# Kernel optimization log

Hardware: AMD Instinct MI355X
Metric: run time of the kernel (lower is better)

The kernel has to match this reference:

```python
import jax, jax.numpy as jnp
import numpy as np

NPOINT = 2048  # N // stride


def sqdist(a, b):
    # a: [B,M,3], b: [B,N,3] -> squared euclidean distances [B,M,N] (== cdist(...)**2)
    return (jnp.sum(a * a, -1)[:, :, None] + jnp.sum(b * b, -1)[:, None, :]
            - 2.0 * jnp.einsum('bmc,bnc->bmn', a, b))


def farthest_point_sample(xyz, npoint):
    # xyz [B,N,3] -> int32 [B,npoint]; deterministic start at point 0
    B, N, _ = xyz.shape

    def step(carry, _):
        distance, farthest = carry
        centroid = jnp.take_along_axis(xyz, farthest[:, None, None], axis=1)  # [B,1,3]
        d = jnp.sum((xyz - centroid) ** 2, -1)                                # [B,N]
        distance = jnp.minimum(distance, d)
        nxt = jnp.argmax(distance, -1).astype(jnp.int32)
        return (distance, nxt), farthest

    init = (jnp.full((B, N), 1e10, xyz.dtype), jnp.zeros((B,), jnp.int32))
    _, idx = jax.lax.scan(step, init, None, length=npoint)
    return idx.T  # [B, npoint]


def ball_query(radius, k, xyz, new_xyz):
    # faithful to torch ball_query: mask out-of-radius as N, sort indices, take first k,
    # replace padding with the first valid neighbor
    B, N, _ = xyz.shape
    sqd = sqdist(new_xyz, xyz)                                   # [B,S,N]
    gi = jnp.where(sqd > radius ** 2, N, jnp.arange(N, dtype=jnp.int32))
    gi = jnp.sort(gi, axis=-1)[:, :, :k]                         # [B,S,k]
    first = gi[:, :, :1]
    return jnp.where(gi == N, first, gi)


def three_interpolation(points, features, query):
    # points [B,S,3], features [B,D,S], query [B,N,3] -> [B,D,N]
    d = sqdist(query, points)                                    # [B,N,S]
    neg, idx = jax.lax.top_k(-d, 3)                              # 3 smallest dists
    w = 1.0 / (-neg + 1e-8)
    w = w / jnp.sum(w, -1, keepdims=True)                        # [B,N,3]
    g = jnp.take_along_axis(features[:, :, None, :], idx[:, None, :, :], axis=3)  # [B,D,N,3]
    return jnp.sum(g * w[:, None, :, :], -1)


def setup_inputs() -> dict:
    key = jax.random.key(0)
    k1, k2, k3, k4 = jax.random.split(key, 4)
    xyz = jax.random.uniform(k1, (4, 8192, 3), dtype=jnp.float32)
    features = jax.random.normal(k2, (4, 64, 8192), dtype=jnp.float32)
    W1 = jax.random.normal(k3, (128, 67), dtype=jnp.float32) * 0.05   # (3+64)->128 pointwise conv
    W2 = jax.random.normal(k4, (128, 192), dtype=jnp.float32) * 0.05  # (64+128)->128 pointwise conv
    return {"xyz": xyz, "features": features, "W1": W1, "W2": W2}


def reference(xyz, features, W1, W2):
    RADIUS, K = 0.2, 16
    # --- set abstraction (SABlock): FPS -> ball query -> group -> conv -> maxpool ---
    sidx = farthest_point_sample(xyz, NPOINT)                        # [B,S]
    new_xyz = jnp.take_along_axis(xyz, sidx[:, :, None], axis=1)     # [B,S,3]
    nidx = ball_query(RADIUS, K, xyz, new_xyz)                       # [B,S,K]
    gxyz = jnp.take_along_axis(xyz[:, None, :, :], nidx[:, :, :, None], axis=2)  # [B,S,K,3]
    rel = gxyz - new_xyz[:, :, None, :]                              # relative coords
    gfeat = jnp.take_along_axis(features[:, :, None, :], nidx[:, None, :, :], axis=3)  # [B,D,S,K]
    grouped = jnp.concatenate([rel.transpose(0, 3, 1, 2), gfeat], axis=1)  # [B,3+D,S,K]
    h = jax.nn.relu(jnp.einsum('od,bdsk->bosk', W1, grouped))
    sub_x = jnp.max(h, -1)                                           # [B,O,S]
    # --- feature propagation (UpBlock): 3-NN interpolation back to N -> concat -> conv ---
    lerp = three_interpolation(new_xyz, sub_x, xyz)                  # [B,O,N]
    cat = jnp.concatenate([features, lerp], axis=1)                  # [B,D+O,N]
    return jax.nn.relu(jnp.einsum('od,bdn->bon', W2, cat))           # [B,O,N]
```

## Files before the change

kernel.cpp:

```cpp
#include <hip/hip_runtime.h>
#include <hip/hip_bf16.h>

#define BATCH 4
#define NPTS  8192
#define NSAMP 2048
#define NK    16
#define CFEAT 64
#define CG    67
#define CO1   128
#define CCAT  192
#define CO2   128

#define DEV __device__ __forceinline__

DEV float n3(float x, float y, float z) {
    return __fadd_rn(__fadd_rn(__fmul_rn(x, x), __fmul_rn(y, y)), __fmul_rn(z, z));
}
DEV float dot3(float ax, float ay, float az, float bx, float by, float bz) {
    return __fmaf_rn(az, bz, __fmaf_rn(ay, by, __fmul_rn(ax, bx)));
}
DEV float sqd_expand(float an, float bn, float d) {
    return __fsub_rn(__fadd_rn(an, bn), __fmul_rn(2.0f, d));
}

__global__ __launch_bounds__(256) void transpose_kernel(const float* __restrict__ F,
                                                        float* __restrict__ T) {
    __shared__ float tile[64][65];
    const int b = blockIdx.y;
    const int n0 = blockIdx.x * 64;
    const int tx = threadIdx.x & 63, ty = threadIdx.x >> 6;
    const float* Fb = F + (size_t)b * CFEAT * NPTS;
    float* Tb = T + (size_t)b * NPTS * CFEAT;
#pragma unroll
    for (int i = 0; i < 16; i++) {
        int c = ty + i * 4;
        tile[c][tx] = Fb[(size_t)c * NPTS + n0 + tx];
    }
    __syncthreads();
#pragma unroll
    for (int i = 0; i < 16; i++) {
        int r = ty + i * 4;
        Tb[(size_t)(n0 + r) * CFEAT + tx] = tile[tx][r];
    }
}

__global__ __launch_bounds__(512) void fps_kernel(const float* __restrict__ xyz,
                                                  float* __restrict__ new_xyz) {
    const int b = blockIdx.x;
    const int t = threadIdx.x;
    const int lane = t & 63, wv = t >> 6;
    const float* X = xyz + (size_t)b * NPTS * 3;

    __shared__ float sx[NPTS], sy[NPTS], sz[NPTS];
    __shared__ unsigned long long wred[2][8];

    float px[16], py[16], pz[16], dist[16];
    {
        const float4* X4 = (const float4*)X;
#pragma unroll
        for (int g = 0; g < 4; g++) {
            float4 f0 = X4[t * 12 + g * 3 + 0];
            float4 f1 = X4[t * 12 + g * 3 + 1];
            float4 f2 = X4[t * 12 + g * 3 + 2];
            px[g*4+0] = f0.x; py[g*4+0] = f0.y; pz[g*4+0] = f0.z;
            px[g*4+1] = f0.w; py[g*4+1] = f1.x; pz[g*4+1] = f1.y;
            px[g*4+2] = f1.z; py[g*4+2] = f1.w; pz[g*4+2] = f2.x;
            px[g*4+3] = f2.y; py[g*4+3] = f2.z; pz[g*4+3] = f2.w;
        }
#pragma unroll
        for (int j = 0; j < 16; j++) {
            int p = t * 16 + j;
            sx[p] = px[j]; sy[p] = py[j]; sz[p] = pz[j];
            dist[j] = 1e10f;
        }
    }
    __syncthreads();

    float cx = sx[0], cy = sy[0], cz = sz[0];
    if (t == 0) {
        size_t o = (size_t)b * NSAMP * 3;
        new_xyz[o + 0] = cx; new_xyz[o + 1] = cy; new_xyz[o + 2] = cz;
    }

    int par = 0;
    for (int s = 1; s < NSAMP; s++) {
#pragma unroll
        for (int j = 0; j < 16; j++) {
            float dx = __fsub_rn(px[j], cx);
            float dy = __fsub_rn(py[j], cy);
            float dz = __fsub_rn(pz[j], cz);
            float d = __fadd_rn(__fadd_rn(__fmul_rn(dx, dx), __fmul_rn(dy, dy)),
                                __fmul_rn(dz, dz));
            dist[j] = fminf(dist[j], d);
        }
        float mx[8];
#pragma unroll
        for (int j = 0; j < 8; j++) mx[j] = fmaxf(dist[2*j], dist[2*j+1]);
#pragma unroll
        for (int j = 0; j < 4; j++) mx[j] = fmaxf(mx[2*j], mx[2*j+1]);
        mx[0] = fmaxf(mx[0], mx[1]);
        float bv = fmaxf(mx[0], fmaxf(mx[2], mx[3]));
        int bj = 15;
#pragma unroll
        for (int j = 14; j >= 0; --j) bj = (dist[j] == bv) ? j : bj;

        float wmax = bv;
#pragma unroll
        for (int off = 32; off > 0; off >>= 1)
            wmax = fmaxf(wmax, __shfl_xor(wmax, off));
        unsigned long long em = __ballot(bv == wmax);
        int wl = __ffsll(em) - 1;
        int lidx = t * 16 + bj;
        int widx = __shfl(lidx, wl);
        if (lane == 0)
            wred[par][wv] = ((unsigned long long)__float_as_uint(wmax) << 32)
                          | (unsigned int)(~widx);
        __syncthreads();

        unsigned long long r0 = wred[par][0], r1 = wred[par][1];
        unsigned long long r2 = wred[par][2], r3 = wred[par][3];
        unsigned long long r4 = wred[par][4], r5 = wred[par][5];
        unsigned long long r6 = wred[par][6], r7 = wred[par][7];
        if (r1 > r0) r0 = r1;
        if (r3 > r2) r2 = r3;
        if (r5 > r4) r4 = r5;
        if (r7 > r6) r6 = r7;
        if (r2 > r0) r0 = r2;
        if (r6 > r4) r4 = r6;
        if (r4 > r0) r0 = r4;
        int idx = (int)(~(unsigned int)(r0 & 0xFFFFFFFFull));

        cx = sx[idx]; cy = sy[idx]; cz = sz[idx];
        if (t == 0) {
            size_t o = ((size_t)b * NSAMP + s) * 3;
            new_xyz[o + 0] = cx; new_xyz[o + 1] = cy; new_xyz[o + 2] = cz;
        }
        par ^= 1;
    }
}

__global__ __launch_bounds__(256) void ballq_kernel(const float* __restrict__ xyz,
                                                    const float* __restrict__ new_xyz,
                                                    int* __restrict__ nidx) {
    const int wv = threadIdx.x >> 6, lane = threadIdx.x & 63;
    const int q = blockIdx.x * 4 + wv;
    const int b = q >> 11;
    const float* X = xyz + (size_t)b * NPTS * 3;
    const float* Q = new_xyz + (size_t)q * 3;
    const float qx = Q[0], qy = Q[1], qz = Q[2];
    const float an = n3(qx, qy, qz);

    __shared__ int nb[4][NK];
    int cnt = 0;
    for (int base = 0; base < NPTS && cnt < NK; base += 64) {
        int p = base + lane;
        float x = X[p * 3 + 0], y = X[p * 3 + 1], z = X[p * 3 + 2];
        float bn = n3(x, y, z);
        float dt = dot3(qx, qy, qz, x, y, z);
        float sq = sqd_expand(an, bn, dt);
        bool in = (sq <= 0.04f);
        unsigned long long m = __ballot(in);
        if (in) {
            int pos = cnt + (int)__popcll(m & ((1ull << lane) - 1ull));
            if (pos < NK) nb[wv][pos] = p;
        }
        cnt += (int)__popcll(m);
    }
    __syncthreads();
    if (lane < NK) {
        int c = cnt < NK ? cnt : NK;
        int v = (lane < c) ? nb[wv][lane] : nb[wv][0];
        nidx[(size_t)q * NK + lane] = v;
    }
}

__global__ __launch_bounds__(256) void group_mlp_kernel(const float* __restrict__ xyz,
                                                        const float* __restrict__ featT,
                                                        const float* __restrict__ new_xyz,
                                                        const int* __restrict__ nidx,
                                                        const float* __restrict__ W1,
                                                        float* __restrict__ subxT) {
    __shared__ float w1t[CG * CO1];
    for (int i = threadIdx.x; i < CG * CO1; i += 256) {
        int d = i >> 7, o = i & 127;
        w1t[i] = W1[(size_t)o * CG + d];
    }
    __syncthreads();
    const int lane = threadIdx.x & 63, wv = threadIdx.x >> 6;

    for (int q = blockIdx.x * 4 + wv; q < BATCH * NSAMP; q += gridDim.x * 4) {
        const int b = q >> 11;
        const float* Q = new_xyz + (size_t)q * 3;
        const float qx = Q[0], qy = Q[1], qz = Q[2];
        const int* NB = nidx + (size_t)q * NK;
        float m0 = 0.0f, m1 = 0.0f;
#pragma unroll 1
        for (int k = 0; k < NK; k++) {
            const int n = NB[k];
            const float* P = xyz + ((size_t)b * NPTS + n) * 3;
            float rx = P[0] - qx, ry = P[1] - qy, rz = P[2] - qz;
            float fv = featT[((size_t)b * NPTS + n) * CFEAT + lane];
            float a0 = fmaf(w1t[0 * CO1 + lane], rx,
                       fmaf(w1t[1 * CO1 + lane], ry, w1t[2 * CO1 + lane] * rz));
            float a1 = fmaf(w1t[0 * CO1 + 64 + lane], rx,
                       fmaf(w1t[1 * CO1 + 64 + lane], ry, w1t[2 * CO1 + 64 + lane] * rz));
#pragma unroll
            for (int d = 3; d < CG; d++) {
                float g = __shfl(fv, d - 3);
                a0 = fmaf(w1t[d * CO1 + lane], g, a0);
                a1 = fmaf(w1t[d * CO1 + 64 + lane], g, a1);
            }
            m0 = fmaxf(m0, a0);
            m1 = fmaxf(m1, a1);
        }
        subxT[(size_t)q * CO1 + lane] = m0;
        subxT[(size_t)q * CO1 + 64 + lane] = m1;
    }
}

DEV void ins3(float dd, int jj,
              float& d0, int& i0, float& d1, int& i1, float& d2, int& i2) {
    bool c2 = (dd < d2) || (dd == d2 && jj < i2);
    if (c2) { d2 = dd; i2 = jj; }
    bool c1 = (d2 < d1) || (d2 == d1 && i2 < i1);
    if (c1) { float tv = d1; int ti = i1; d1 = d2; i1 = i2; d2 = tv; i2 = ti; }
    bool c0 = (d1 < d0) || (d1 == d0 && i1 < i0);
    if (c0) { float tv = d0; int ti = i0; d0 = d1; i0 = i1; d1 = tv; i1 = ti; }
}

__global__ __launch_bounds__(256) void interp_w2_kernel(const float* __restrict__ xyz,
                                                        const float* __restrict__ new_xyz,
                                                        const float* __restrict__ featT,
                                                        const float* __restrict__ subxT,
                                                        const float* __restrict__ W2,
                                                        float* __restrict__ out) {
    __shared__ float w2t[CCAT * CO2];
    __shared__ float catb[4][CCAT];
    for (int i = threadIdx.x; i < CCAT * CO2; i += 256) {
        int d = i >> 7, o = i & 127;
        w2t[i] = W2[(size_t)o * CCAT + d];
    }
    __syncthreads();
    const int lane = threadIdx.x & 63, wv = threadIdx.x >> 6;

    for (int q = blockIdx.x * 4 + wv; q < BATCH * NPTS; q += gridDim.x * 4) {
        const int b = q >> 13, n = q & (NPTS - 1);
        const float* P = xyz + (size_t)q * 3;
        const float qx = P[0], qy = P[1], qz = P[2];
        const float an = n3(qx, qy, qz);

        float d0 = 1e30f, d1 = 1e30f, d2 = 1e30f;
        int i0 = 0x7fffffff, i1 = 0x7fffffff, i2 = 0x7fffffff;
        for (int j = lane; j < NSAMP; j += 64) {
            const float* C = new_xyz + ((size_t)b * NSAMP + j) * 3;
            float x = C[0], y = C[1], z = C[2];
            float bn = n3(x, y, z);
            float dt = dot3(qx, qy, qz, x, y, z);
            float dd = sqd_expand(an, bn, dt);
            ins3(dd, j, d0, i0, d1, i1, d2, i2);
        }
#pragma unroll
        for (int off = 32; off > 0; off >>= 1) {
            float e0 = __shfl_xor(d0, off); int f0 = __shfl_xor(i0, off);
            float e1 = __shfl_xor(d1, off); int f1 = __shfl_xor(i1, off);
            float e2 = __shfl_xor(d2, off); int f2 = __shfl_xor(i2, off);
            ins3(e0, f0, d0, i0, d1, i1, d2, i2);
            ins3(e1, f1, d0, i0, d1, i1, d2, i2);
            ins3(e2, f2, d0, i0, d1, i1, d2, i2);
        }
        float w0 = 1.0f / (d0 + 1e-8f);
        float w1 = 1.0f / (d1 + 1e-8f);
        float w2 = 1.0f / (d2 + 1e-8f);
        float sw = (w0 + w1) + w2;
        w0 /= sw; w1 /= sw; w2 /= sw;

        const float* S = subxT + (size_t)b * NSAMP * CO1;
        float L0 = S[(size_t)i0 * CO1 + lane] * w0
                 + S[(size_t)i1 * CO1 + lane] * w1
                 + S[(size_t)i2 * CO1 + lane] * w2;
        float L1 = S[(size_t)i0 * CO1 + 64 + lane] * w0
                 + S[(size_t)i1 * CO1 + 64 + lane] * w1
                 + S[(size_t)i2 * CO1 + 64 + lane] * w2;

        float fv = featT[((size_t)b * NPTS + n) * CFEAT + lane];
        catb[wv][lane] = fv;
        catb[wv][64 + lane] = L0;
        catb[wv][128 + lane] = L1;
        __builtin_amdgcn_s_waitcnt(0);

        float a0 = 0.0f, a1 = 0.0f;
#pragma unroll 8
        for (int d = 0; d < CCAT; d++) {
            float cv = catb[wv][d];
            a0 = fmaf(w2t[d * CO2 + lane], cv, a0);
            a1 = fmaf(w2t[d * CO2 + 64 + lane], cv, a1);
        }
        out[((size_t)b * CO2 + lane) * NPTS + n] = fmaxf(a0, 0.0f);
        out[((size_t)b * CO2 + 64 + lane) * NPTS + n] = fmaxf(a1, 0.0f);
    }
}

extern "C" void kernel_launch(void* const* d_in, const int* in_sizes, int n_in,
                              void* d_out, int out_size, void* d_ws, size_t ws_size,
                              hipStream_t stream) {
    const float* xyz      = (const float*)d_in[0];
    const float* features = (const float*)d_in[1];
    const float* W1       = (const float*)d_in[2];
    const float* W2       = (const float*)d_in[3];
    float* out = (float*)d_out;

    float* featT   = (float*)d_ws;
    float* new_xyz = featT + (size_t)BATCH * NPTS * CFEAT;
    int*   nidx    = (int*)(new_xyz + (size_t)BATCH * NSAMP * 3);
    float* subxT   = (float*)(nidx + (size_t)BATCH * NSAMP * NK);

    transpose_kernel<<<dim3(NPTS / 64, BATCH), 256, 0, stream>>>(features, featT);
    fps_kernel<<<BATCH, 512, 0, stream>>>(xyz, new_xyz);
    ballq_kernel<<<(BATCH * NSAMP) / 4, 256, 0, stream>>>(xyz, new_xyz, nidx);
    group_mlp_kernel<<<512, 256, 0, stream>>>(xyz, featT, new_xyz, nidx, W1, subxT);
    interp_w2_kernel<<<256, 256, 0, stream>>>(xyz, new_xyz, featT, subxT, W2, out);
}
```

Measured before the change: 2.834 ms.

## Spatially sort FPS points into grid cells and cull distance updates by bounding sphere

Points are bucketed into an 8x8x8 grid with a shared-memory counting sort, so each thread owns 16 spatially nearby points. Each thread keeps a bounding sphere and its current max min-distance, and skips the distance update when the new centroid is too far away to lower any of its distances. Whole waves whose lanes all skip reuse their cached packed max instead of redoing the shuffle reduction. This trades a one-time sort plus extra branches and registers for less per-iteration arithmetic in the serial FPS loop. Tie-breaking now takes the minimum original index through pid, which should preserve argmax semantics.

```diff
diff --git a/kernel.cpp b/kernel.cpp
--- a/kernel.cpp
+++ b/kernel.cpp
@@ -23,6 +23,13 @@
     return __fsub_rn(__fadd_rn(an, bn), __fmul_rn(2.0f, d));
 }
 
+DEV int cellof(float x, float y, float z) {
+    int ix = min(7, (int)(x * 8.0f));
+    int iy = min(7, (int)(y * 8.0f));
+    int iz = min(7, (int)(z * 8.0f));
+    return (iz << 6) | (iy << 3) | ix;
+}
+
 __global__ __launch_bounds__(256) void transpose_kernel(const float* __restrict__ F,
                                                         float* __restrict__ T) {
     __shared__ float tile[64][65];
@@ -52,9 +59,13 @@
     const float* X = xyz + (size_t)b * NPTS * 3;
 
     __shared__ float sx[NPTS], sy[NPTS], sz[NPTS];
+    __shared__ unsigned short sidx[NPTS];
+    __shared__ unsigned int cnt_off[512];
     __shared__ unsigned long long wred[2][8];
 
     float px[16], py[16], pz[16], dist[16];
+    int pid[16];
+
     {
         const float4* X4 = (const float4*)X;
 #pragma unroll
@@ -71,10 +82,58 @@
         for (int j = 0; j < 16; j++) {
             int p = t * 16 + j;
             sx[p] = px[j]; sy[p] = py[j]; sz[p] = pz[j];
-            dist[j] = 1e10f;
-        }
-    }
-    __syncthreads();
+        }
+    }
+    cnt_off[t] = 0;
+    __syncthreads();
+#pragma unroll
+    for (int j = 0; j < 16; j++)
+        atomicAdd(&cnt_off[cellof(px[j], py[j], pz[j])], 1u);
+    __syncthreads();
+    if (t < 64) {
+        unsigned h[8], lsum = 0;
+#pragma unroll
+        for (int k = 0; k < 8; k++) { h[k] = cnt_off[t * 8 + k]; lsum += h[k]; }
+        unsigned run = lsum;
+#pragma unroll
+        for (int d = 1; d < 64; d <<= 1) {
+            unsigned o = __shfl_up(run, d);
+            if (lane >= d) run += o;
+        }
+        unsigned acc = run - lsum;
+#pragma unroll
+        for (int k = 0; k < 8; k++) { cnt_off[t * 8 + k] = acc; acc += h[k]; }
+    }
+    __syncthreads();
+#pragma unroll
+    for (int j = 0; j < 16; j++) {
+        int c = cellof(px[j], py[j], pz[j]);
+        unsigned pos = atomicAdd(&cnt_off[c], 1u);
+        sidx[pos] = (unsigned short)(t * 16 + j);
+    }
+    __syncthreads();
+#pragma unroll
+    for (int j = 0; j < 16; j++) {
+        int p = sidx[t * 16 + j];
+        pid[j] = p;
+        px[j] = sx[p]; py[j] = sy[p]; pz[j] = sz[p];
+        dist[j] = 1e10f;
+    }
+    float mnx = px[0], mxx = px[0], mny = py[0], mxy = py[0], mnz = pz[0], mxz = pz[0];
+#pragma unroll
+    for (int j = 1; j < 16; j++) {
+        mnx = fminf(mnx, px[j]); mxx = fmaxf(mxx, px[j]);
+        mny = fminf(mny, py[j]); mxy = fmaxf(mxy, py[j]);
+        mnz = fminf(mnz, pz[j]); mxz = fmaxf(mxz, pz[j]);
+    }
+    const float rx = 0.5f * (mnx + mxx), ry = 0.5f * (mny + mxy), rz = 0.5f * (mnz + mxz);
+    float r2m = 0.0f;
+#pragma unroll
+    for (int j = 0; j < 16; j++) {
+        float dx = px[j] - rx, dy = py[j] - ry, dz = pz[j] - rz;
+        r2m = fmaxf(r2m, dx * dx + dy * dy + dz * dz);
+    }
+    const float rad = sqrtf(r2m) * 1.0001f + 1e-6f;
 
     float cx = sx[0], cy = sy[0], cz = sz[0];
     if (t == 0) {
@@ -82,39 +141,52 @@
         new_xyz[o + 0] = cx; new_xyz[o + 1] = cy; new_xyz[o + 2] = cz;
     }
 
+    float bv = 1e10f;
+    int bidx = 0;
+    float cullR = 3e38f;
+    unsigned long long wpack = 0;
+
     int par = 0;
     for (int s = 1; s < NSAMP; s++) {
-#pragma unroll
-        for (int j = 0; j < 16; j++) {
-            float dx = __fsub_rn(px[j], cx);
-            float dy = __fsub_rn(py[j], cy);
-            float dz = __fsub_rn(pz[j], cz);
-            float d = __fadd_rn(__fadd_rn(__fmul_rn(dx, dx), __fmul_rn(dy, dy)),
-                                __fmul_rn(dz, dz));
-            dist[j] = fminf(dist[j], d);
-        }
-        float mx[8];
-#pragma unroll
-        for (int j = 0; j < 8; j++) mx[j] = fmaxf(dist[2*j], dist[2*j+1]);
-#pragma unroll
-        for (int j = 0; j < 4; j++) mx[j] = fmaxf(mx[2*j], mx[2*j+1]);
-        mx[0] = fmaxf(mx[0], mx[1]);
-        float bv = fmaxf(mx[0], fmaxf(mx[2], mx[3]));
-        int bj = 15;
-#pragma unroll
-        for (int j = 14; j >= 0; --j) bj = (dist[j] == bv) ? j : bj;
-
-        float wmax = bv;
-#pragma unroll
-        for (int off = 32; off > 0; off >>= 1)
-            wmax = fmaxf(wmax, __shfl_xor(wmax, off));
-        unsigned long long em = __ballot(bv == wmax);
-        int wl = __ffsll(em) - 1;
-        int lidx = t * 16 + bj;
-        int widx = __shfl(lidx, wl);
-        if (lane == 0)
-            wred[par][wv] = ((unsigned long long)__float_as_uint(wmax) << 32)
-                          | (unsigned int)(~widx);
+        float ddx = cx - rx, ddy = cy - ry, ddz = cz - rz;
+        float dc2 = ddx * ddx + ddy * ddy + ddz * ddz;
+        bool upd = dc2 < cullR;
+        if (__ballot(upd) != 0) {
+            if (upd) {
+#pragma unroll
+                for (int j = 0; j < 16; j++) {
+                    float dx = __fsub_rn(px[j], cx);
+                    float dy = __fsub_rn(py[j], cy);
+                    float dz = __fsub_rn(pz[j], cz);
+                    float d = __fadd_rn(__fadd_rn(__fmul_rn(dx, dx), __fmul_rn(dy, dy)),
+                                        __fmul_rn(dz, dz));
+                    dist[j] = fminf(dist[j], d);
+                }
+                float m8[8];
+#pragma unroll
+                for (int j = 0; j < 8; j++) m8[j] = fmaxf(dist[j], dist[j + 8]);
+#pragma unroll
+                for (int j = 0; j < 4; j++) m8[j] = fmaxf(m8[j], m8[j + 4]);
+                bv = fmaxf(fmaxf(m8[0], m8[1]), fmaxf(m8[2], m8[3]));
+                int nb = 0x7fffffff;
+#pragma unroll
+                for (int j = 0; j < 16; j++)
+                    if (dist[j] == bv) nb = min(nb, pid[j]);
+                bidx = nb;
+                float sb = sqrtf(bv) * 1.0001f + 1e-6f;
+                float rr = rad + sb;
+                cullR = rr * rr;
+            }
+            unsigned long long pk = ((unsigned long long)__float_as_uint(bv) << 32)
+                                  | (unsigned int)(~bidx);
+#pragma unroll
+            for (int off = 32; off > 0; off >>= 1) {
+                unsigned long long o = __shfl_xor(pk, off);
+                if (o > pk) pk = o;
+            }
+            wpack = pk;
+        }
+        if (lane == 0) wred[par][wv] = wpack;
         __syncthreads();
 
         unsigned long long r0 = wred[par][0], r1 = wred[par][1];
```

Result: slower. 3.768 ms (+33.0%).
